# Kernel tuning notes

Measured on AMD Instinct MI355X. Metric: run time of the kernel, lower is better.

Reference implementation:

```python
import jax, jax.numpy as jnp
import numpy as np

B, C, H, W = 8, 512, 64, 64
IC = C // 2  # inter_channel


def setup_inputs() -> dict:
    key = jax.random.key(0)
    ks = jax.random.split(key, 10)
    s = 0.02
    return {
        "x": jax.random.normal(ks[0], (B, C, H, W), dtype=jnp.float32),
        "y": jax.random.normal(ks[1], (B, C, H, W), dtype=jnp.float32),
        "w_phi": jax.random.normal(ks[2], (IC, C), dtype=jnp.float32) * s,
        "b_phi": jnp.zeros((IC,), dtype=jnp.float32),
        "w_theta": jax.random.normal(ks[3], (IC, C), dtype=jnp.float32) * s,
        "b_theta": jnp.zeros((IC,), dtype=jnp.float32),
        "w_g": jax.random.normal(ks[4], (IC, C), dtype=jnp.float32) * s,
        "b_g": jnp.zeros((IC,), dtype=jnp.float32),
        "w_mask": jax.random.normal(ks[5], (C, IC), dtype=jnp.float32) * s,
        "b_mask": jnp.zeros((C,), dtype=jnp.float32),
    }


def _conv1x1(w, b, t):
    # t: [b, cin, h, w]; 1x1 conv == channel matmul
    return jnp.einsum('oc,bchw->bohw', w, t) + b[None, :, None, None]


def reference(x, y, w_phi, b_phi, w_theta, b_theta, w_g, b_g, w_mask, b_mask):
    b, c, h, w = x.shape
    ic = w_phi.shape[0]  # c // 2
    # Faithful to the torch code: conv outputs ic channels but is viewed as
    # (b, c, -1), so the sequence length is N = h*w//2 and feature dim is c.
    x_phi = _conv1x1(w_phi, b_phi, y).reshape(b, c, -1)              # [b, c, N]
    x_theta = _conv1x1(w_theta, b_theta, x).reshape(b, c, -1)
    x_theta = jnp.transpose(x_theta, (0, 2, 1))                      # [b, N, c]
    x_g = _conv1x1(w_g, b_g, x).reshape(b, c, -1)
    dict
    x_g = jnp.transpose(x_g, (0, 2, 1))                              # [b, N, c]
    scores = jnp.einsum('bnc,bcm->bnm', x_theta, x_phi)              # [b, N, N]
    attn = jax.nn.softmax(scores, axis=1)  # softmax over dim=1 (columns), as in torch
    out_nl = jnp.einsum('bnm,bmc->bnc', attn, x_g)                   # [b, N, c]
    out_nl = jnp.transpose(out_nl, (0, 2, 1)).reshape(b, ic, h, w)   # [b, ic, h, w]
    mask = _conv1x1(w_mask, b_mask, out_nl)                          # [b, c, h, w]
    return mask + x
```

## Files before the change

### kernel.cpp

```cpp
#include <hip/hip_runtime.h>
#include <hip/hip_bf16.h>


typedef __attribute__((ext_vector_type(8))) short short8;
typedef __attribute__((ext_vector_type(4))) short short4v;
typedef __attribute__((ext_vector_type(4))) float f32x4;

enum { EPI_BF16 = 0, EPI_BF16_BIAS = 1 };

__device__ __forceinline__ short f2bf(float f) {
  union { __hip_bfloat16 h; short s; } u; u.h = __float2bfloat16(f); return u.s;
}
__device__ __forceinline__ float bf2f(short s) {
  union { short s; __hip_bfloat16 h; } u; u.s = s; return __bfloat162float(u.h);
}

__device__ __forceinline__ void async_ld16(const void* g, void* l) {
  __builtin_amdgcn_global_load_lds(
      (const __attribute__((address_space(1))) unsigned int*)(unsigned long long)g,
      (__attribute__((address_space(3))) unsigned int*)(unsigned int)(unsigned long long)l,
      16, 0, 0);
}

template<int EPI>
__global__ __launch_bounds__(512, 4)
void gemm8(const short* __restrict__ Ag, long sA, int lda,
           const short* __restrict__ Bg, long sB, int ldb,
           short* __restrict__ Cg, long sC, int ldc,
           int K, const float* __restrict__ bias)
{
  __shared__ __align__(16) short As[128 * 32];
  __shared__ __align__(16) short Bs[128 * 32];
  const int bz = blockIdx.z;
  const short* A = Ag + (long)bz * sA;
  const short* B = Bg + (long)bz * sB;
  const int m0 = blockIdx.y * 128;
  const int n0 = blockIdx.x * 128;
  const int t = threadIdx.x;
  const int wv = t >> 6, ln = t & 63;
  const int wr = wv >> 1, wc = wv & 1;
  const int fr = ln & 15, q8 = (ln >> 4) * 8;
  const int rowA = t >> 2, kc = (t & 3) * 8;

  f32x4 acc[2][4];
  #pragma unroll
  for (int i = 0; i < 2; i++)
    #pragma unroll
    for (int j = 0; j < 4; j++)
      #pragma unroll
      for (int r = 0; r < 4; r++) acc[i][j][r] = 0.f;

  for (int kk = 0; kk < K; kk += 32) {
    async_ld16(A + (long)(m0 + rowA) * lda + kk + kc, As + wv * 512);
    async_ld16(B + (long)(n0 + rowA) * ldb + kk + kc, Bs + wv * 512);
    __syncthreads();
    short8 af[2], bfr[4];
    #pragma unroll
    for (int mi = 0; mi < 2; mi++) af[mi] = *(const short8*)&As[(wr * 32 + mi * 16 + fr) * 32 + q8];
    #pragma unroll
    for (int ni = 0; ni < 4; ni++) bfr[ni] = *(const short8*)&Bs[(wc * 64 + ni * 16 + fr) * 32 + q8];
    #pragma unroll
    for (int mi = 0; mi < 2; mi++)
      #pragma unroll
      for (int ni = 0; ni < 4; ni++)
        acc[mi][ni] = __builtin_amdgcn_mfma_f32_16x16x32_bf16(af[mi], bfr[ni], acc[mi][ni], 0, 0, 0);
    __syncthreads();
  }

  const int colb = n0 + wc * 64 + fr;
  const int rowb = m0 + wr * 32 + (ln >> 4) * 4;
  #pragma unroll
  for (int mi = 0; mi < 2; mi++)
    #pragma unroll
    for (int r = 0; r < 4; r++) {
      const int mr = rowb + mi * 16 + r;
      float badd = 0.f;
      if constexpr (EPI == EPI_BF16_BIAS) badd = bias[mr];
      #pragma unroll
      for (int ni = 0; ni < 4; ni++)
        Cg[(long)bz * sC + (long)mr * ldc + colb + ni * 16] = f2bf(acc[mi][ni][r] + badd);
    }
}

__global__ __launch_bounds__(512, 4)
void ov_k(const short* __restrict__ Eg, const short* __restrict__ Gg,
          short* __restrict__ Cg)
{
  const int L = blockIdx.x;
  const int xcd = L & 7, k = L >> 3;
  const int slab = xcd + ((k >> 2) << 3);
  const int bz = slab >> 4, by = slab & 15, bx = k & 3;

  __shared__ __align__(16) short As[128 * 32];
  __shared__ __align__(16) short Bs[128 * 32];
  const short* A = Eg + ((long)bz << 22);
  const short* B = Gg + ((long)bz << 20);
  const int m0 = by * 128;
  const int n0 = bx * 128;
  const int t = threadIdx.x;
  const int wv = t >> 6, ln = t & 63;
  const int wr = wv >> 1, wc = wv & 1;
  const int fr = ln & 15, q8 = (ln >> 4) * 8;
  const int rowA = t >> 2, kc = (t & 3) * 8;

  f32x4 acc[2][4];
  #pragma unroll
  for (int i = 0; i < 2; i++)
    #pragma unroll
    for (int j = 0; j < 4; j++)
      #pragma unroll
      for (int r = 0; r < 4; r++) acc[i][j][r] = 0.f;

  for (int kk = 0; kk < 2048; kk += 32) {
    async_ld16(A + (long)(m0 + rowA) * 2048 + kk + kc, As + wv * 512);
    async_ld16(B + (long)(n0 + rowA) * 2048 + kk + kc, Bs + wv * 512);
    __syncthreads();
    short8 af[2], bfr[4];
    #pragma unroll
    for (int mi = 0; mi < 2; mi++) af[mi] = *(const short8*)&As[(wr * 32 + mi * 16 + fr) * 32 + q8];
    #pragma unroll
    for (int ni = 0; ni < 4; ni++) bfr[ni] = *(const short8*)&Bs[(wc * 64 + ni * 16 + fr) * 32 + q8];
    #pragma unroll
    for (int mi = 0; mi < 2; mi++)
      #pragma unroll
      for (int ni = 0; ni < 4; ni++)
        acc[mi][ni] = __builtin_amdgcn_mfma_f32_16x16x32_bf16(af[mi], bfr[ni], acc[mi][ni], 0, 0, 0);
    __syncthreads();
  }

  const int colb = n0 + wc * 64 + fr;
  const int rowb = m0 + wr * 32 + (ln >> 4) * 4;
  #pragma unroll
  for (int mi = 0; mi < 2; mi++)
    #pragma unroll
    for (int r = 0; r < 4; r++) {
      const int mr = rowb + mi * 16 + r;
      #pragma unroll
      for (int ni = 0; ni < 4; ni++)
        Cg[((long)bz << 20) + (long)mr * 512 + colb + ni * 16] = f2bf(acc[mi][ni][r]);
    }
}

__global__ __launch_bounds__(256)
void conv_pt(const short* __restrict__ imgT,
             const short* __restrict__ wth, const short* __restrict__ wph,
             const float* __restrict__ bth, const float* __restrict__ bph,
             short* __restrict__ TPT2)
{
  __shared__ __align__(16) short As[128 * 32];
  __shared__ __align__(16) short Bs[128 * 32];
  const int m0 = blockIdx.y * 128;
  const int n0 = blockIdx.x * 128;
  const bool isphi = blockIdx.y >= 256;
  const short* A = imgT + (long)m0 * 512;
  const short* B = isphi ? wph : wth;
  const float* bias = isphi ? bph : bth;
  const int t = threadIdx.x;
  const int wv = t >> 6, ln = t & 63;
  const int wm = (wv >> 1) * 64, wn = (wv & 1) * 64;
  const int fr = ln & 15, q8 = (ln >> 4) * 8;
  const int rowA = t >> 2, kc = (t & 3) * 8;

  f32x4 acc[4][4];
  #pragma unroll
  for (int i = 0; i < 4; i++)
    #pragma unroll
    for (int j = 0; j < 4; j++)
      #pragma unroll
      for (int r = 0; r < 4; r++) acc[i][j][r] = 0.f;

  for (int kk = 0; kk < 512; kk += 32) {
    #pragma unroll
    for (int s = 0; s < 2; s++) {
      async_ld16(A + (long)(s * 64 + rowA) * 512 + kk + kc, As + (s * 256 + wv * 64) * 8);
      async_ld16(B + (long)(n0 + s * 64 + rowA) * 512 + kk + kc, Bs + (s * 256 + wv * 64) * 8);
    }
    __syncthreads();
    short8 af[4], bfr[4];
    #pragma unroll
    for (int mi = 0; mi < 4; mi++) af[mi] = *(const short8*)&As[(wm + mi * 16 + fr) * 32 + q8];
    #pragma unroll
    for (int ni = 0; ni < 4; ni++) bfr[ni] = *(const short8*)&Bs[(wn + ni * 16 + fr) * 32 + q8];
    #pragma unroll
    for (int mi = 0; mi < 4; mi++)
      #pragma unroll
      for (int ni = 0; ni < 4; ni++)
        acc[mi][ni] = __builtin_amdgcn_mfma_f32_16x16x32_bf16(af[mi], bfr[ni], acc[mi][ni], 0, 0, 0);
    __syncthreads();
  }

  const int colb = n0 + wn + fr;
  const int rowb = m0 + wm + (ln >> 4) * 4;
  float cb[4];
  #pragma unroll
  for (int ni = 0; ni < 4; ni++) cb[ni] = bias[colb + ni * 16];
  #pragma unroll
  for (int mi = 0; mi < 4; mi++)
    #pragma unroll
    for (int r = 0; r < 4; r++) {
      const long mr = rowb + mi * 16 + r;
      #pragma unroll
      for (int ni = 0; ni < 4; ni++)
        TPT2[mr * 256 + colb + ni * 16] = f2bf(acc[mi][ni][r] + cb[ni]);
    }
}

__global__ __launch_bounds__(256)
void scores_k(const short* __restrict__ TT2, const short* __restrict__ PT2,
              short* __restrict__ ST, float* __restrict__ pstats)
{
  __shared__ __align__(16) short As[128 * 32];
  __shared__ __align__(16) short Bs[128 * 32];
  const int bz = blockIdx.z, by = blockIdx.y, bx = blockIdx.x;
  const int t = threadIdx.x;
  const int wv = t >> 6, ln = t & 63;
  const int wm = (wv >> 1) * 64, wn = (wv & 1) * 64;
  const int fr = ln & 15, q8 = (ln >> 4) * 8;
  const int rowA = t >> 2, kc = (t & 3) * 8;

  f32x4 acc[4][4];
  #pragma unroll
  for (int i = 0; i < 4; i++)
    #pragma unroll
    for (int j = 0; j < 4; j++)
      #pragma unroll
      for (int r = 0; r < 4; r++) acc[i][j][r] = 0.f;

  #pragma unroll
  for (int h = 0; h < 2; h++) {
    const short* Aseg = TT2 + ((long)(bz * 4096 + h * 2048 + by * 128)) * 256;
    const short* Bseg = PT2 + ((long)(bz * 4096 + h * 2048 + bx * 128)) * 256;
    for (int kk = 0; kk < 256; kk += 32) {
      #pragma unroll
      for (int s = 0; s < 2; s++) {
        async_ld16(Aseg + (long)(s * 64 + rowA) * 256 + kk + kc, As + (s * 256 + wv * 64) * 8);
        async_ld16(Bseg + (long)(s * 64 + rowA) * 256 + kk + kc, Bs + (s * 256 + wv * 64) * 8);
      }
      __syncthreads();
      short8 af[4], bfr[4];
      #pragma unroll
      for (int mi = 0; mi < 4; mi++) af[mi] = *(const short8*)&As[(wm + mi * 16 + fr) * 32 + q8];
      #pragma unroll
      for (int ni = 0; ni < 4; ni++) bfr[ni] = *(const short8*)&Bs[(wn + ni * 16 + fr) * 32 + q8];
      #pragma unroll
      for (int mi = 0; mi < 4; mi++)
        #pragma unroll
        for (int ni = 0; ni < 4; ni++)
          acc[mi][ni] = __builtin_amdgcn_mfma_f32_16x16x32_bf16(af[mi], bfr[ni], acc[mi][ni], 0, 0, 0);
      __syncthreads();
    }
  }

  const int colb = bx * 128 + wn + fr;
  const int rowb = by * 128 + wm + (ln >> 4) * 4;
  short* base = ST + ((long)bz << 22);
  float ps[4] = {0.f, 0.f, 0.f, 0.f};
  #pragma unroll
  for (int mi = 0; mi < 4; mi++)
    #pragma unroll
    for (int r = 0; r < 4; r++) {
      const long mr = rowb + mi * 16 + r;
      #pragma unroll
      for (int ni = 0; ni < 4; ni++) {
        float e = __expf(acc[mi][ni][r]);
        base[mr * 2048 + colb + ni * 16] = f2bf(e);
        ps[ni] += e;
      }
    }
  #pragma unroll
  for (int ni = 0; ni < 4; ni++) {
    ps[ni] += __shfl_xor(ps[ni], 16);
    ps[ni] += __shfl_xor(ps[ni], 32);
  }
  float* part = (float*)As;
  if (ln < 16) {
    #pragma unroll
    for (int ni = 0; ni < 4; ni++)
      part[(wv >> 1) * 128 + wn + ni * 16 + fr] = ps[ni];
  }
  __syncthreads();
  if (t < 128)
    pstats[((long)(bz * 16 + by)) * 2048 + bx * 128 + t] = part[t] + part[128 + t];
}

__global__ __launch_bounds__(256)
void zfinal(const float* __restrict__ pstats, float* __restrict__ invZ)
{
  const int g = blockIdx.x * 256 + threadIdx.x;
  const int b = g >> 11, col = g & 2047;
  float S = 0.f;
  #pragma unroll
  for (int rc = 0; rc < 16; rc++) S += pstats[((long)(b * 16 + rc)) * 2048 + col];
  invZ[g] = 1.f / S;
}

__global__ __launch_bounds__(256)
void g_scale(short* __restrict__ G, const float* __restrict__ invZ)
{
  const long base = ((long)blockIdx.x * 256 + threadIdx.x) * 8;
  const int bz = (int)(base >> 20);
  const int n2 = (int)(base & 4095);
  const float* z = invZ + bz * 2048 + (n2 & 2047);
  short8 v = *(short8*)&G[base];
  f32x4 z0 = *(const f32x4*)z;
  f32x4 z1 = *(const f32x4*)(z + 4);
  #pragma unroll
  for (int j = 0; j < 4; j++) { v[j] = f2bf(bf2f(v[j]) * z0[j]); v[4 + j] = f2bf(bf2f(v[4 + j]) * z1[j]); }
  *(short8*)&G[base] = v;
}

__global__ __launch_bounds__(256)
void mask_k(const short* __restrict__ Wm20, const short* __restrict__ Wm21,
            const short* __restrict__ OVT, const float* __restrict__ bmask,
            const float* __restrict__ x, float* __restrict__ out)
{
  __shared__ __align__(16) short As[128 * 32];
  __shared__ __align__(16) short Bs[128 * 32];
  const int bz = blockIdx.z;
  const int n0 = blockIdx.x * 128;
  const int m0 = blockIdx.y * 128;
  const short* A = (n0 >= 2048) ? Wm21 : Wm20;
  const short* B = OVT + ((long)bz << 20) + (long)(n0 & 2047) * 512;
  const int t = threadIdx.x;
  const int wv = t >> 6, ln = t & 63;
  const int wm = (wv >> 1) * 64, wn = (wv & 1) * 64;
  const int fr = ln & 15, q8 = (ln >> 4) * 8;
  const int rowA = t >> 2, kc = (t & 3) * 8;

  f32x4 acc[4][4];
  #pragma unroll
  for (int i = 0; i < 4; i++)
    #pragma unroll
    for (int j = 0; j < 4; j++)
      #pragma unroll
      for (int r = 0; r < 4; r++) acc[i][j][r] = 0.f;

  for (int kk = 0; kk < 512; kk += 32) {
    #pragma unroll
    for (int s = 0; s < 2; s++) {
      async_ld16(A + (long)(m0 + s * 64 + rowA) * 512 + kk + kc, As + (s * 256 + wv * 64) * 8);
      async_ld16(B + (long)(s * 64 + rowA) * 512 + kk + kc, Bs + (s * 256 + wv * 64) * 8);
    }
    __syncthreads();
    short8 af[4], bfr[4];
    #pragma unroll
    for (int mi = 0; mi < 4; mi++) af[mi] = *(const short8*)&As[(wm + mi * 16 + fr) * 32 + q8];
    #pragma unroll
    for (int ni = 0; ni < 4; ni++) bfr[ni] = *(const short8*)&Bs[(wn + ni * 16 + fr) * 32 + q8];
    #pragma unroll
    for (int mi = 0; mi < 4; mi++)
      #pragma unroll
      for (int ni = 0; ni < 4; ni++)
        acc[mi][ni] = __builtin_amdgcn_mfma_f32_16x16x32_bf16(af[mi], bfr[ni], acc[mi][ni], 0, 0, 0);
    __syncthreads();
  }

  const int colb = n0 + wn + fr;
  const int rowb = m0 + wm + (ln >> 4) * 4;
  #pragma unroll
  for (int mi = 0; mi < 4; mi++)
    #pragma unroll
    for (int r = 0; r < 4; r++) {
      const int mr = rowb + mi * 16 + r;
      const float badd = bmask[mr];
      const long rbase = ((long)bz * 512 + mr) * 4096;
      #pragma unroll
      for (int ni = 0; ni < 4; ni++) {
        const int cc = colb + ni * 16;
        out[rbase + cc] = acc[mi][ni][r] + badd + x[rbase + cc];
      }
    }
}

__global__ __launch_bounds__(256)
void wconv2(const float* w_phi, const float* w_theta, const float* w_g,
            const float* w_mask,
            short* wph, short* wth, short* wg, short* Wm20, short* Wm21)
{
  const int seg = blockIdx.x >> 6;
  const int blk = blockIdx.x & 63;
  const int i0 = blk * 2048 + threadIdx.x * 8;
  if (seg < 3) {
    const float* s = seg == 0 ? w_phi : seg == 1 ? w_theta : w_g;
    short* d = seg == 0 ? wph : seg == 1 ? wth : wg;
    f32x4 a = *(const f32x4*)&s[i0];
    f32x4 b = *(const f32x4*)&s[i0 + 4];
    short8 o;
    #pragma unroll
    for (int j = 0; j < 4; j++) { o[j] = f2bf(a[j]); o[4 + j] = f2bf(b[j]); }
    *(short8*)&d[i0] = o;
  } else {
    const int o = i0 >> 8;
    f32x4 a = *(const f32x4*)&w_mask[i0];
    f32x4 b = *(const f32x4*)&w_mask[i0 + 4];
    short v[8];
    #pragma unroll
    for (int j = 0; j < 4; j++) { v[j] = f2bf(a[j]); v[4 + j] = f2bf(b[j]); }
    short8 a0, a1, b0, b1;
    #pragma unroll
    for (int j = 0; j < 4; j++) {
      a0[2 * j] = v[j];     a0[2 * j + 1] = 0;
      a1[2 * j] = v[4 + j]; a1[2 * j + 1] = 0;
      b0[2 * j] = 0;        b0[2 * j + 1] = v[j];
      b1[2 * j] = 0;        b1[2 * j + 1] = v[4 + j];
    }
    const long base = (long)o * 512 + 2 * (i0 & 255);
    *(short8*)&Wm20[base] = a0; *(short8*)&Wm20[base + 8] = a1;
    *(short8*)&Wm21[base] = b0; *(short8*)&Wm21[base + 8] = b1;
  }
}

__global__ __launch_bounds__(256)
void convtr(const float* __restrict__ x, const float* __restrict__ y,
            short* __restrict__ xT, short* __restrict__ yT)
{
  __shared__ __align__(16) short Ts[64 * 136];
  const int z = blockIdx.z;
  const float* src = (z < 8 ? x : y) + (long)(z & 7) * 512 * 4096;
  short* dst = (z < 8 ? xT : yT) + (long)(z & 7) * 4096 * 512;
  const int c0 = blockIdx.y * 128;
  const int n0 = blockIdx.x * 64;
  const int t = threadIdx.x;

  const int i16 = t & 15;
  const int rbase = t >> 4;
  const int sw = (i16 & 3) << 3;
  f32x4 v[8];
  #pragma unroll
  for (int p = 0; p < 8; p++)
    v[p] = *(const f32x4*)&src[(long)(c0 + p * 16 + rbase) * 4096 + n0 + i16 * 4];
  #pragma unroll
  for (int p = 0; p < 8; p++) {
    const int c = p * 16 + rbase;
    const int cs = c ^ sw;
    #pragma unroll
    for (int j = 0; j < 4; j++)
      Ts[(i16 * 4 + j) * 136 + cs] = f2bf(v[p][j]);
  }
  __syncthreads();

  #pragma unroll
  for (int q = 0; q < 4; q++) {
    const int idx = q * 256 + t;
    const int px = idx >> 4;
    const int p16 = idx & 15;
    const int sw2 = ((px >> 2) & 3) << 3;
    short8 o = *(const short8*)&Ts[px * 136 + ((p16 * 8) ^ sw2)];
    *(short8*)&dst[(long)(n0 + px) * 512 + c0 + p16 * 8] = o;
  }
}

extern "C" void kernel_launch(void* const* d_in, const int* in_sizes, int n_in,
                              void* d_out, int out_size, void* d_ws, size_t ws_size,
                              hipStream_t stream)
{
  (void)in_sizes; (void)n_in; (void)out_size; (void)ws_size;
  const float* x       = (const float*)d_in[0];
  const float* y       = (const float*)d_in[1];
  const float* w_phi   = (const float*)d_in[2];
  const float* b_phi   = (const float*)d_in[3];
  const float* w_theta = (const float*)d_in[4];
  const float* b_theta = (const float*)d_in[5];
  const float* w_g     = (const float*)d_in[6];
  const float* b_g     = (const float*)d_in[7];
  const float* w_mask  = (const float*)d_in[8];
  const float* b_mask  = (const float*)d_in[9];
  float* out = (float*)d_out;

  char* ws = (char*)d_ws;
  const long MB = 1L << 20;
  short* wph  = (short*)(ws + 0);
  short* wth  = (short*)(ws + 256 * 1024);
  short* wg   = (short*)(ws + 512 * 1024);
  short* Wm20 = (short*)(ws + 768 * 1024);
  short* Wm21 = (short*)(ws + 1280 * 1024);
  short* xT   = (short*)(ws + 2 * MB);
  short* yT   = (short*)(ws + 34 * MB);
  short* TPT2 = (short*)(ws + 66 * MB);
  short* G    = (short*)(ws + 98 * MB);
  short* ST   = (short*)(ws + 2 * MB);
  float* pstats = (float*)(ws + 114 * MB);
  float* invZ   = (float*)(ws + 115 * MB);
  short* OVT  = (short*)(ws + 66 * MB);

  dim3 blk(256, 1, 1);
  dim3 blk8(512, 1, 1);

  wconv2<<<dim3(256, 1, 1), blk, 0, stream>>>(w_phi, w_theta, w_g, w_mask,
                                              wph, wth, wg, Wm20, Wm21);
  convtr<<<dim3(64, 4, 16), blk, 0, stream>>>(x, y, xT, yT);

  conv_pt<<<dim3(2, 512, 1), blk, 0, stream>>>(xT, wth, wph, b_theta, b_phi, TPT2);

  gemm8<EPI_BF16_BIAS><<<dim3(32, 2, 8), blk8, 0, stream>>>(
      wg, 0, 512, xT, 4096L * 512, 512, G, 1048576L, 4096, 512, b_g);

  scores_k<<<dim3(16, 16, 8), blk, 0, stream>>>(TPT2, TPT2 + 32768L * 256, ST, pstats);
  zfinal<<<dim3(64, 1, 1), blk, 0, stream>>>(pstats, invZ);
  g_scale<<<dim3(4096, 1, 1), blk, 0, stream>>>(G, invZ);

  ov_k<<<dim3(512, 1, 1), blk8, 0, stream>>>(ST, G, OVT);

  mask_k<<<dim3(32, 4, 8), blk, 0, stream>>>(Wm20, Wm21, OVT, b_mask, x, out);
}
```

Before: 396.3 us.

## Fuse fp32-to-bf16 transpose into theta/phi and g projection GEMM loads

Removes the separate convtr kernel that wrote bf16 transposed copies of x and y. The conv_ptf and new gemmG_f kernels now read fp32 x/y directly, convert and transpose them into swizzled LDS tiles inside the K loop. The g projection is also retiled to cover all 256 output rows per block. This drops a full write and re-read of the transposed activations and one launch. In exchange, each GEMM block issues synchronous fp32 global loads instead of async LDS copies, which may stall the main loop, and x is read from fp32 twice.

```diff
diff --git a/kernel.cpp b/kernel.cpp
--- a/kernel.cpp
+++ b/kernel.cpp
@@ -22,64 +22,28 @@
       16, 0, 0);
 }
 
-template<int EPI>
-__global__ __launch_bounds__(512, 4)
-void gemm8(const short* __restrict__ Ag, long sA, int lda,
-           const short* __restrict__ Bg, long sB, int ldb,
-           short* __restrict__ Cg, long sC, int ldc,
-           int K, const float* __restrict__ bias)
-{
-  __shared__ __align__(16) short As[128 * 32];
-  __shared__ __align__(16) short Bs[128 * 32];
-  const int bz = blockIdx.z;
-  const short* A = Ag + (long)bz * sA;
-  const short* B = Bg + (long)bz * sB;
-  const int m0 = blockIdx.y * 128;
-  const int n0 = blockIdx.x * 128;
-  const int t = threadIdx.x;
-  const int wv = t >> 6, ln = t & 63;
-  const int wr = wv >> 1, wc = wv & 1;
-  const int fr = ln & 15, q8 = (ln >> 4) * 8;
-  const int rowA = t >> 2, kc = (t & 3) * 8;
-
-  f32x4 acc[2][4];
-  #pragma unroll
-  for (int i = 0; i < 2; i++)
-    #pragma unroll
-    for (int j = 0; j < 4; j++)
-      #pragma unroll
-      for (int r = 0; r < 4; r++) acc[i][j][r] = 0.f;
-
-  for (int kk = 0; kk < K; kk += 32) {
-    async_ld16(A + (long)(m0 + rowA) * lda + kk + kc, As + wv * 512);
-    async_ld16(B + (long)(n0 + rowA) * ldb + kk + kc, Bs + wv * 512);
-    __syncthreads();
-    short8 af[2], bfr[4];
-    #pragma unroll
-    for (int mi = 0; mi < 2; mi++) af[mi] = *(const short8*)&As[(wr * 32 + mi * 16 + fr) * 32 + q8];
-    #pragma unroll
-    for (int ni = 0; ni < 4; ni++) bfr[ni] = *(const short8*)&Bs[(wc * 64 + ni * 16 + fr) * 32 + q8];
-    #pragma unroll
-    for (int mi = 0; mi < 2; mi++)
-      #pragma unroll
-      for (int ni = 0; ni < 4; ni++)
-        acc[mi][ni] = __builtin_amdgcn_mfma_f32_16x16x32_bf16(af[mi], bfr[ni], acc[mi][ni], 0, 0, 0);
-    __syncthreads();
-  }
-
-  const int colb = n0 + wc * 64 + fr;
-  const int rowb = m0 + wr * 32 + (ln >> 4) * 4;
-  #pragma unroll
-  for (int mi = 0; mi < 2; mi++)
-    #pragma unroll
-    for (int r = 0; r < 4; r++) {
-      const int mr = rowb + mi * 16 + r;
-      float badd = 0.f;
-      if constexpr (EPI == EPI_BF16_BIAS) badd = bias[mr];
-      #pragma unroll
-      for (int ni = 0; ni < 4; ni++)
-        Cg[(long)bz * sC + (long)mr * ldc + colb + ni * 16] = f2bf(acc[mi][ni][r] + badd);
-    }
+__device__ __forceinline__ void stage_tr(const float* __restrict__ src,
+                                         int kk, int px0, int s, short* Ds)
+{
+  const int g4 = (s >> 5) * 4;
+  const int p4 = (s & 31) * 4;
+  f32x4 v0 = *(const f32x4*)&src[(long)(kk + g4 + 0) * 4096 + px0 + p4];
+  f32x4 v1 = *(const f32x4*)&src[(long)(kk + g4 + 1) * 4096 + px0 + p4];
+  f32x4 v2 = *(const f32x4*)&src[(long)(kk + g4 + 2) * 4096 + px0 + p4];
+  f32x4 v3 = *(const f32x4*)&src[(long)(kk + g4 + 3) * 4096 + px0 + p4];
+  #pragma unroll
+  for (int j = 0; j < 4; j++) {
+    short4v w;
+    w[0] = f2bf(v0[j]); w[1] = f2bf(v1[j]); w[2] = f2bf(v2[j]); w[3] = f2bf(v3[j]);
+    const int px = p4 + j;
+    const int u = (g4 >> 3) ^ ((px >> 2) & 3);
+    *(short4v*)&Ds[px * 32 + u * 8 + (g4 & 4)] = w;
+  }
+}
+
+__device__ __forceinline__ short8 frag_sw(const short* Ds, int row, int q8)
+{
+  return *(const short8*)&Ds[row * 32 + (((q8 >> 3) ^ ((row >> 2) & 3)) << 3)];
 }
 
 __global__ __launch_bounds__(512, 4)
@@ -142,17 +106,18 @@
 }
 
 __global__ __launch_bounds__(256)
-void conv_pt(const short* __restrict__ imgT,
-             const short* __restrict__ wth, const short* __restrict__ wph,
-             const float* __restrict__ bth, const float* __restrict__ bph,
-             short* __restrict__ TPT2)
+void conv_ptf(const float* __restrict__ x, const float* __restrict__ y,
+              const short* __restrict__ wth, const short* __restrict__ wph,
+              const float* __restrict__ bth, const float* __restrict__ bph,
+              short* __restrict__ TPT2)
 {
   __shared__ __align__(16) short As[128 * 32];
   __shared__ __align__(16) short Bs[128 * 32];
   const int m0 = blockIdx.y * 128;
   const int n0 = blockIdx.x * 128;
   const bool isphi = blockIdx.y >= 256;
-  const short* A = imgT + (long)m0 * 512;
+  const float* src = (isphi ? y : x) + ((long)((m0 >> 12) & 7)) * (512L * 4096);
+  const int px0 = m0 & 4095;
   const short* B = isphi ? wph : wth;
   const float* bias = isphi ? bph : bth;
   const int t = threadIdx.x;
@@ -171,14 +136,13 @@
 
   for (int kk = 0; kk < 512; kk += 32) {
     #pragma unroll
-    for (int s = 0; s < 2; s++) {
-      async_ld16(A + (long)(s * 64 + rowA) * 512 + kk + kc, As + (s * 256 + wv * 64) * 8);
+    for (int s = 0; s < 2; s++)
       async_ld16(B + (long)(n0 + s * 64 + rowA) * 512 + kk + kc, Bs + (s * 256 + wv * 64) * 8);
-    }
+    stage_tr(src, kk, px0, t, As);
     __syncthreads();
     short8 af[4], bfr[4];
     #pragma unroll
-    for (int mi = 0; mi < 4; mi++) af[mi] = *(const short8*)&As[(wm + mi * 16 + fr) * 32 + q8];
+    for (int mi = 0; mi < 4; mi++) af[mi] = frag_sw(As, wm + mi * 16 + fr, q8);
     #pragma unroll
     for (int ni = 0; ni < 4; ni++) bfr[ni] = *(const short8*)&Bs[(wn + ni * 16 + fr) * 32 + q8];
     #pragma unroll
@@ -202,6 +166,61 @@
       #pragma unroll
       for (int ni = 0; ni < 4; ni++)
         TPT2[mr * 256 + colb + ni * 16] = f2bf(acc[mi][ni][r] + cb[ni]);
+    }
+}
+
+__global__ __launch_bounds__(512, 2)
+void gemmG_f(const float* __restrict__ x, const short* __restrict__ wg,
+             const float* __restrict__ bg, short* __restrict__ G)
+{
+  __shared__ __align__(16) short As[256 * 32];
+  __shared__ __align__(16) short Bs[128 * 32];
+  const int img = blockIdx.y;
+  const int n0 = blockIdx.x * 128;
+  const float* src = x + (long)img * 512 * 4096;
+  const int t = threadIdx.x;
+  const int wv = t >> 6, ln = t & 63;
+  const int wr = wv >> 1, wc = wv & 1;
+  const int fr = ln & 15, q8 = (ln >> 4) * 8;
+  const int rowA = t >> 2, kc = (t & 3) * 8;
+
+  f32x4 acc[4][4];
+  #pragma unroll
+  for (int i = 0; i < 4; i++)
+    #pragma unroll
+    for (int j = 0; j < 4; j++)
+      #pragma unroll
+      for (int r = 0; r < 4; r++) acc[i][j][r] = 0.f;
+
+  for (int kk = 0; kk < 512; kk += 32) {
+    async_ld16(wg + (long)rowA * 512 + kk + kc, As + wv * 512);
+    async_ld16(wg + (long)(128 + rowA) * 512 + kk + kc, As + 4096 + wv * 512);
+    if (t < 256) stage_tr(src, kk, n0, t, Bs);
+    __syncthreads();
+    short8 af[4], bfr[4];
+    #pragma unroll
+    for (int mi = 0; mi < 4; mi++) af[mi] = *(const short8*)&As[(wr * 64 + mi * 16 + fr) * 32 + q8];
+    #pragma unroll
+    for (int ni = 0; ni < 4; ni++) bfr[ni] = frag_sw(Bs, wc * 64 + ni * 16 + fr, q8);
+    #pragma unroll
+    for (int mi = 0; mi < 4; mi++)
+      #pragma unroll
+      for (int ni = 0; ni < 4; ni++)
+        acc[mi][ni] = __builtin_amdgcn_mfma_f32_16x16x32_bf16(af[mi], bfr[ni], acc[mi][ni], 0, 0, 0);
+    __syncthreads();
+  }
+
+  const int colb = n0 + wc * 64 + fr;
+  const int rowb = wr * 64 + (ln >> 4) * 4;
+  #pragma unroll
+  for (int mi = 0; mi < 4; mi++)
+    #pragma unroll
+    for (int r = 0; r < 4; r++) {
+      const int mr = rowb + mi * 16 + r;
+      const float badd = bg[mr];
+      #pragma unroll
+      for (int ni = 0; ni < 4; ni++)
+        G[((long)img << 20) + (long)mr * 4096 + colb + ni * 16] = f2bf(acc[mi][ni][r] + badd);
     }
 }
 
@@ -410,46 +429,6 @@
   }
 }
 
-__global__ __launch_bounds__(256)
-void convtr(const float* __restrict__ x, const float* __restrict__ y,
-            short* __restrict__ xT, short* __restrict__ yT)
-{
-  __shared__ __align__(16) short Ts[64 * 136];
-  const int z = blockIdx.z;
-  const float* src = (z < 8 ? x : y) + (long)(z & 7) * 512 * 4096;
-  short* dst = (z < 8 ? xT : yT) + (long)(z & 7) * 4096 * 512;
-  const int c0 = blockIdx.y * 128;
-  const int n0 = blockIdx.x * 64;
-  const int t = threadIdx.x;
-
-  const int i16 = t & 15;
-  const int rbase = t >> 4;
-  const int sw = (i16 & 3) << 3;
-  f32x4 v[8];
-  #pragma unroll
-  for (int p = 0; p < 8; p++)
-    v[p] = *(const f32x4*)&src[(long)(c0 + p * 16 + rbase) * 4096 + n0 + i16 * 4];
-  #pragma unroll
-  for (int p = 0; p < 8; p++) {
-    const int c = p * 16 + rbase;
-    const int cs = c ^ sw;
-    #pragma unroll
-    for (int j = 0; j < 4; j++)
-      Ts[(i16 * 4 + j) * 136 + cs] = f2bf(v[p][j]);
-  }
-  __syncthreads();
-
-  #pragma unroll
-  for (int q = 0; q < 4; q++) {
-    const int idx = q * 256 + t;
-    const int px = idx >> 4;
-    const int p16 = idx & 15;
-    const int sw2 = ((px >> 2) & 3) << 3;
-    short8 o = *(const short8*)&Ts[px * 136 + ((p16 * 8) ^ sw2)];
-    *(short8*)&dst[(long)(n0 + px) * 512 + c0 + p16 * 8] = o;
-  }
-}
-
 extern "C" void kernel_launch(void* const* d_in, const int* in_sizes, int n_in,
                               void* d_out, int out_size, void* d_ws, size_t ws_size,
                               hipStream_t stream)
@@ -474,8 +453,6 @@
   short* wg   = (short*)(ws + 512 * 1024);
   short* Wm20 = (short*)(ws + 768 * 1024);
   short* Wm21 = (short*)(ws + 1280 * 1024);
-  short* xT   = (short*)(ws + 2 * MB);
-  short* yT   = (short*)(ws + 34 * MB);
   short* TPT2 = (short*)(ws + 66 * MB);
   short* G    = (short*)(ws + 98 * MB);
   short* ST   = (short*)(ws + 2 * MB);
@@ -488,12 +465,10 @@
 
   wconv2<<<dim3(256, 1, 1), blk, 0, stream>>>(w_phi, w_theta, w_g, w_mask,
                                               wph, wth, wg, Wm20, Wm21);
-  convtr<<<dim3(64, 4, 16), blk, 0, stream>>>(x, y, xT, yT);
-
-  conv_pt<<<dim3(2, 512, 1), blk, 0, stream>>>(xT, wth, wph, b_theta, b_phi, TPT2);
-
-  gemm8<EPI_BF16_BIAS><<<dim3(32, 2, 8), blk8, 0, stream>>>(
-      wg, 0, 512, xT, 4096L * 512, 512, G, 1048576L, 4096, 512, b_g);
+
+  conv_ptf<<<dim3(2, 512, 1), blk, 0, stream>>>(x, y, wth, wph, b_theta, b_phi, TPT2);
+
+  gemmG_f<<<dim3(32, 8, 1), blk8, 0, stream>>>(x, wg, b_g, G);
 
   scores_k<<<dim3(16, 16, 8), blk, 0, stream>>>(TPT2, TPT2 + 32768L * 256, ST, pstats);
   zfinal<<<dim3(64, 1, 1), blk, 0, stream>>>(pstats, invZ);
```

Result: faster. 375.5 us (-5.2%).
